# Performance work log

Hardware: AMD Instinct MI355X
Metric: run time of the kernel (lower is better)

Reference implementation:

```python
import jax, jax.numpy as jnp
import numpy as np
import math

B, S, DIM, HEADS, HEAD_DIM = 2, 2048, 1024, 16, 64
ROT_DIM, ROPE_THETA = 64, 10000.0


def make_rope(seq_len):
    # DitRotary.forward: theta over half rotary_dim, duplicated interleaved pairs
    theta = 1.0 / (ROPE_THETA ** (np.arange(0, ROT_DIM, 2, dtype=np.float32) / ROT_DIM))
    pos = np.arange(seq_len, dtype=np.float32).reshape(-1, 1)
    idx = pos * theta  # [S, 32]
    cos = np.stack((np.cos(idx), np.cos(idx)), axis=-1).reshape(seq_len, -1)  # [S, 64]
    sin = np.stack((np.sin(idx), np.sin(idx)), axis=-1).reshape(seq_len, -1)
    # unsqueeze(2).unsqueeze(1) -> [1, S, 1, 64]
    return jnp.asarray(cos)[None, :, None, :], jnp.asarray(sin)[None, :, None, :]


def rotate_half(x):
    # interleaved-pair rotation: (x1, x2) -> (-x2, x1)
    x = x.reshape(*x.shape[:-1], -1, 2)
    x1, x2 = x[..., 0], x[..., 1]
    return jnp.stack((-x2, x1), axis=-1).reshape(*x.shape[:-2], -1)


def apply_rotary(x, cos, sin):
    return x * cos + rotate_half(x) * sin


def setup_inputs() -> dict:
    key = jax.random.key(0)
    ks = jax.random.split(key, 8)
    sc = 1.0 / math.sqrt(DIM)
    x = jax.random.normal(ks[0], (B, S, DIM), dtype=jnp.float32)
    cos, sin = make_rope(S)
    Wq = jax.random.normal(ks[1], (DIM, DIM), dtype=jnp.float32) * sc
    bq = jnp.zeros((DIM,), jnp.float32)
    Wk = jax.random.normal(ks[2], (DIM, DIM), dtype=jnp.float32) * sc
    bk = jnp.zeros((DIM,), jnp.float32)
    Wv = jax.random.normal(ks[3], (DIM, DIM), dtype=jnp.float32) * sc
    bv = jnp.zeros((DIM,), jnp.float32)
    Wo = jax.random.normal(ks[4], (DIM, DIM), dtype=jnp.float32) * sc
    bo = jnp.zeros((DIM,), jnp.float32)
    mask = jnp.ones((B, 1, 1, S), dtype=bool)
    return {"x": x, "cos": cos, "sin": sin, "Wq": Wq, "bq": bq, "Wk": Wk,
            "bk": bk, "Wv": Wv, "bv": bv, "Wo": Wo, "bo": bo, "mask": mask}


def reference(x, cos, sin, Wq, bq, Wk, bk, Wv, bv, Wo, bo, mask):
    b, s, _ = x.shape
    q = (x @ Wq.T + bq).reshape(b, s, HEADS, HEAD_DIM)
    k = (x @ Wk.T + bk).reshape(b, s, HEADS, HEAD_DIM)
    v = (x @ Wv.T + bv).reshape(b, s, HEADS, HEAD_DIM)
    # partial rotary: applied only to head index 0 (dim 2 of [B,S,H,D])
    q = jnp.concatenate([apply_rotary(q[:, :, :1, :], cos, sin), q[:, :, 1:, :]], axis=2)
    k = jnp.concatenate([apply_rotary(k[:, :, :1, :], cos, sin), k[:, :, 1:, :]], axis=2)
    # [B,H,S,D]
    q = q.transpose(0, 2, 1, 3)
    k = k.transpose(0, 2, 1, 3)
    v = v.transpose(0, 2, 1, 3)
    neg = jnp.finfo(jnp.float32).min
    attn_mask = jnp.where(mask, 0.0, neg)  # ~mask * finfo.min
    scores = jnp.einsum("bhsd,bhtd->bhst", q, k) / math.sqrt(HEAD_DIM)
    scores = scores + attn_mask
    probs = jax.nn.softmax(scores.astype(jnp.float32), axis=-1).astype(q.dtype)
    out = jnp.einsum("bhst,bhtd->bhsd", probs, v)
    out = out.transpose(0, 2, 1, 3).reshape(b, s, HEADS * HEAD_DIM)
    return out @ Wo.T + bo
```

## Files before the change

### kernel.cpp

```cpp
#include <hip/hip_runtime.h>
#include <hip/hip_bf16.h>


typedef __attribute__((ext_vector_type(8))) __bf16 bf16x8;
typedef __attribute__((ext_vector_type(4))) __bf16 bf16x4;
typedef __attribute__((ext_vector_type(4))) float f32x4;
typedef __attribute__((ext_vector_type(4))) short s16x4;

#define NB_B 2
#define NB_S 2048
#define NB_DIM 1024
#define NB_H 16
#define NB_HD 64
#define NB_BS (NB_B * NB_S)

__device__ __forceinline__ void async_cp16(const __bf16* g, __bf16* l) {
    __builtin_amdgcn_global_load_lds(
        (const __attribute__((address_space(1))) unsigned int*)g,
        (__attribute__((address_space(3))) unsigned int*)l, 16, 0, 0);
}

__global__ __launch_bounds__(256) void cvt_kernel(
    const float* __restrict__ x,  const float* __restrict__ wq,
    const float* __restrict__ wk, const float* __restrict__ wv,
    const float* __restrict__ wo,
    __bf16* __restrict__ xb,  __bf16* __restrict__ wqb,
    __bf16* __restrict__ wkb, __bf16* __restrict__ wvb,
    __bf16* __restrict__ wob) {
    const int XQ = (NB_BS * NB_DIM) / 4;
    const int WQ = (NB_DIM * NB_DIM) / 4;
    int i = blockIdx.x * 256 + threadIdx.x;
    const float* src; __bf16* dst; int off;
    if (i < XQ)              { src = x;  dst = xb;  off = i; }
    else if (i < XQ + WQ)    { src = wq; dst = wqb; off = i - XQ; }
    else if (i < XQ + 2*WQ)  { src = wk; dst = wkb; off = i - XQ - WQ; }
    else if (i < XQ + 3*WQ)  { src = wv; dst = wvb; off = i - XQ - 2*WQ; }
    else                     { src = wo; dst = wob; off = i - XQ - 3*WQ; }
    f32x4 v = *(const f32x4*)(src + (size_t)off * 4);
    bf16x4 b;
#pragma unroll
    for (int j = 0; j < 4; ++j) b[j] = (__bf16)v[j];
    *(bf16x4*)(dst + (size_t)off * 4) = b;
}

__global__ __launch_bounds__(256) void gemm_qkv_kernel(
    const __bf16* __restrict__ A,
    const float* __restrict__ cosb, const float* __restrict__ sinb,
    const __bf16* __restrict__ Wq, const float* __restrict__ bq, __bf16* __restrict__ qbuf,
    const __bf16* __restrict__ Wk, const float* __restrict__ bk, __bf16* __restrict__ kbuf,
    const __bf16* __restrict__ Wv, const float* __restrict__ bv, __bf16* __restrict__ vtbuf) {
    constexpr int K = 1024;
    constexpr int NT = K / 32;
    __shared__ __align__(16) __bf16 As[3][128][32];
    __shared__ __align__(16) __bf16 Bs[3][128][32];

    const int z = blockIdx.z;
    const __bf16* W; const float* bias;
    if (z == 0)      { W = Wq; bias = bq; }
    else if (z == 1) { W = Wk; bias = bk; }
    else             { W = Wv; bias = bv; }

    const int tid = threadIdx.x;
    const int lane = tid & 63;
    const int w = tid >> 6;
    const int wm = w >> 1, wn = w & 1;
    const int row16 = lane & 15, quad = lane >> 4;
    const int m0 = blockIdx.x * 128, n0 = blockIdx.y * 128;

    f32x4 acc[4][4] = {};

    auto stage = [&](int nb, int kt) {
#pragma unroll
        for (int i = 0; i < 2; ++i) {
            int c = tid + i * 256;
            int row = c >> 2;
            int co = (c & 3) << 3;
            async_cp16(A + (size_t)(m0 + row) * K + kt + co, &As[nb][row][co]);
            async_cp16(W + (size_t)(n0 + row) * K + kt + co, &Bs[nb][row][co]);
        }
    };
    auto compute = [&](int nb) {
        bf16x8 af[4], bfr[4];
#pragma unroll
        for (int t = 0; t < 4; ++t) {
            af[t]  = *(const bf16x8*)&As[nb][wm * 64 + t * 16 + row16][quad * 8];
            bfr[t] = *(const bf16x8*)&Bs[nb][wn * 64 + t * 16 + row16][quad * 8];
        }
        __builtin_amdgcn_s_setprio(1);
#pragma unroll
        for (int mt = 0; mt < 4; ++mt)
#pragma unroll
            for (int nt = 0; nt < 4; ++nt)
                acc[mt][nt] = __builtin_amdgcn_mfma_f32_16x16x32_bf16(af[mt], bfr[nt], acc[mt][nt], 0, 0, 0);
        __builtin_amdgcn_s_setprio(0);
    };

    stage(0, 0);
    stage(1, 32);
    int cu = 0, pfb = 2;
    for (int t = 0; t < NT - 1; ++t) {
        asm volatile("s_waitcnt vmcnt(4)" ::: "memory");
        __builtin_amdgcn_s_barrier();
        if (t + 2 < NT) stage(pfb, (t + 2) * 32);
        compute(cu);
        cu  = (cu  == 2) ? 0 : cu + 1;
        pfb = (pfb == 2) ? 0 : pfb + 1;
    }
    asm volatile("s_waitcnt vmcnt(0)" ::: "memory");
    __builtin_amdgcn_s_barrier();
    compute(cu);

    if (z == 2) {
#pragma unroll
        for (int mt = 0; mt < 4; ++mt) {
            int row = m0 + wm * 64 + mt * 16 + quad * 4;
            int b = row >> 11, s = row & (NB_S - 1);
#pragma unroll
            for (int nt = 0; nt < 4; ++nt) {
                int col = n0 + wn * 64 + nt * 16 + row16;
                float bv = bias[col];
                bf16x4 pack;
#pragma unroll
                for (int r = 0; r < 4; ++r) pack[r] = (__bf16)(acc[mt][nt][r] + bv);
                *(bf16x4*)&vtbuf[(size_t)b * (NB_DIM * NB_S) + (size_t)col * NB_S + s] = pack;
            }
        }
    } else {
        __bf16* C = (z == 0) ? qbuf : kbuf;
        const bool rope = (n0 == 0) && (wn == 0);
#pragma unroll
        for (int mt = 0; mt < 4; ++mt) {
            int row = m0 + wm * 64 + mt * 16 + quad * 4;
#pragma unroll
            for (int nt = 0; nt < 4; ++nt) {
                int col = n0 + wn * 64 + nt * 16 + row16;
                float bv = bias[col];
#pragma unroll
                for (int r = 0; r < 4; ++r) {
                    float val = acc[mt][nt][r] + bv;
                    if (rope) {
                        float part = __shfl_xor(val, 1, 64);
                        int srow = (row + r) & (NB_S - 1);
                        float c  = cosb[srow * 64 + col];
                        float sn = sinb[srow * 64 + col];
                        val = (lane & 1) ? (val * c + part * sn) : (val * c - part * sn);
                    }
                    C[(size_t)(row + r) * NB_DIM + col] = (__bf16)val;
                }
            }
        }
    }
}

__global__ __launch_bounds__(256) void gemm_o_kernel(
    const __bf16* __restrict__ A, const __bf16* __restrict__ W,
    const float* __restrict__ bias, float* __restrict__ C) {
    constexpr int K = 1024;
    constexpr int NT = K / 32;
    __shared__ __align__(16) __bf16 As[3][128][32];
    __shared__ __align__(16) __bf16 Bs[3][64][32];

    const int tid = threadIdx.x;
    const int lane = tid & 63;
    const int w = tid >> 6;
    const int row16 = lane & 15, quad = lane >> 4;
    const int m0 = blockIdx.x * 128, n0 = blockIdx.y * 64;

    f32x4 acc[2][4] = {};

    auto stage = [&](int nb, int kt) {
#pragma unroll
        for (int i = 0; i < 2; ++i) {
            int c = tid + i * 256;
            int row = c >> 2;
            int co = (c & 3) << 3;
            async_cp16(A + (size_t)(m0 + row) * K + kt + co, &As[nb][row][co]);
        }
        {
            int row = tid >> 2;
            int co = (tid & 3) << 3;
            async_cp16(W + (size_t)(n0 + row) * K + kt + co, &Bs[nb][row][co]);
        }
    };
    auto compute = [&](int nb) {
        bf16x8 af[2], bfr[4];
#pragma unroll
        for (int t = 0; t < 2; ++t)
            af[t] = *(const bf16x8*)&As[nb][w * 32 + t * 16 + row16][quad * 8];
#pragma unroll
        for (int nt = 0; nt < 4; ++nt)
            bfr[nt] = *(const bf16x8*)&Bs[nb][nt * 16 + row16][quad * 8];
        __builtin_amdgcn_s_setprio(1);
#pragma unroll
        for (int mt = 0; mt < 2; ++mt)
#pragma unroll
            for (int nt = 0; nt < 4; ++nt)
                acc[mt][nt] = __builtin_amdgcn_mfma_f32_16x16x32_bf16(af[mt], bfr[nt], acc[mt][nt], 0, 0, 0);
        __builtin_amdgcn_s_setprio(0);
    };

    stage(0, 0);
    stage(1, 32);
    int cu = 0, pfb = 2;
    for (int t = 0; t < NT - 1; ++t) {
        asm volatile("s_waitcnt vmcnt(3)" ::: "memory");
        __builtin_amdgcn_s_barrier();
        if (t + 2 < NT) stage(pfb, (t + 2) * 32);
        compute(cu);
        cu  = (cu  == 2) ? 0 : cu + 1;
        pfb = (pfb == 2) ? 0 : pfb + 1;
    }
    asm volatile("s_waitcnt vmcnt(0)" ::: "memory");
    __builtin_amdgcn_s_barrier();
    compute(cu);

#pragma unroll
    for (int mt = 0; mt < 2; ++mt) {
        int row = m0 + w * 32 + mt * 16 + quad * 4;
#pragma unroll
        for (int nt = 0; nt < 4; ++nt) {
            int col = n0 + nt * 16 + row16;
            float bv = bias[col];
#pragma unroll
            for (int r = 0; r < 4; ++r)
                C[(size_t)(row + r) * NB_DIM + col] = acc[mt][nt][r] + bv;
        }
    }
}

__global__ __launch_bounds__(256) void attn_kernel(const __bf16* __restrict__ qb,
                                                   const __bf16* __restrict__ kb,
                                                   const __bf16* __restrict__ vtb,
                                                   __bf16* __restrict__ ob) {
    __shared__ __align__(16) __bf16 Ks[128][72];
    __shared__ __align__(16) __bf16 Vts[64][132];

    const int tid = threadIdx.x;
    const int lane = tid & 63;
    const int w = tid >> 6;
    const int row16 = lane & 15, quad = lane >> 4;
    const int bh = blockIdx.y;
    const int b = bh >> 4, h = bh & 15;
    const int q0 = blockIdx.x * 128 + w * 32;

    const size_t headoff = (size_t)b * NB_S * NB_DIM + (size_t)h * NB_HD;
    const size_t vtoff = (size_t)b * (NB_DIM * NB_S) + (size_t)(h * NB_HD) * NB_S;

    const float qscale = 0.18033688011112042f;
    bf16x8 qf[2][2];
#pragma unroll
    for (int m = 0; m < 2; ++m)
#pragma unroll
        for (int hh = 0; hh < 2; ++hh) {
            bf16x8 v = *(const bf16x8*)(qb + headoff + (size_t)(q0 + m * 16 + row16) * NB_DIM + hh * 32 + quad * 8);
#pragma unroll
            for (int j = 0; j < 8; ++j) v[j] = (__bf16)((float)v[j] * qscale);
            qf[m][hh] = v;
        }

    f32x4 o[2][4] = {};
    f32x4 ol[2] = {};

    const short one_bf16 = (short)0x3F80;
    const s16x4 onesf = {one_bf16, one_bf16, one_bf16, one_bf16};

    bf16x8 kreg[4], vreg[4];
#pragma unroll
    for (int i = 0; i < 4; ++i) {
        int c = tid + i * 256;
        kreg[i] = *(const bf16x8*)(kb + headoff + (size_t)(c >> 3) * NB_DIM + ((c & 7) << 3));
        vreg[i] = *(const bf16x8*)(vtb + vtoff + (size_t)(c >> 4) * NB_S + ((c & 15) << 3));
    }

    for (int kt = 0; kt < 16; ++kt) {
        __syncthreads();
#pragma unroll
        for (int i = 0; i < 4; ++i) {
            int c = tid + i * 256;
            *(bf16x8*)&Ks[c >> 3][(c & 7) << 3] = kreg[i];
            bf16x4 lo, hi;
#pragma unroll
            for (int j = 0; j < 4; ++j) { lo[j] = vreg[i][j]; hi[j] = vreg[i][j + 4]; }
            *(bf16x4*)&Vts[c >> 4][(c & 15) << 3] = lo;
            *(bf16x4*)&Vts[c >> 4][((c & 15) << 3) + 4] = hi;
        }
        __syncthreads();
        if (kt < 15) {
            int base = (kt + 1) * 128;
#pragma unroll
            for (int i = 0; i < 4; ++i) {
                int c = tid + i * 256;
                kreg[i] = *(const bf16x8*)(kb + headoff + (size_t)(base + (c >> 3)) * NB_DIM + ((c & 7) << 3));
                vreg[i] = *(const bf16x8*)(vtb + vtoff + (size_t)(c >> 4) * NB_S + base + ((c & 15) << 3));
            }
        }

        s16x4 pf[2][8];
#pragma unroll
        for (int t = 0; t < 8; ++t) {
            f32x4 s0 = {}, s1 = {};
            __builtin_amdgcn_s_setprio(1);
#pragma unroll
            for (int hh = 0; hh < 2; ++hh) {
                bf16x8 kf = *(const bf16x8*)&Ks[t * 16 + row16][hh * 32 + quad * 8];
                s0 = __builtin_amdgcn_mfma_f32_16x16x32_bf16(kf, qf[0][hh], s0, 0, 0, 0);
                s1 = __builtin_amdgcn_mfma_f32_16x16x32_bf16(kf, qf[1][hh], s1, 0, 0, 0);
            }
            __builtin_amdgcn_s_setprio(0);
            bf16x4 p0, p1;
#pragma unroll
            for (int r = 0; r < 4; ++r) {
                float e0 = __builtin_amdgcn_exp2f(s0[r]); p0[r] = (__bf16)e0;
                float e1 = __builtin_amdgcn_exp2f(s1[r]); p1[r] = (__bf16)e1;
            }
            pf[0][t] = __builtin_bit_cast(s16x4, p0);
            pf[1][t] = __builtin_bit_cast(s16x4, p1);
            ol[0] = __builtin_amdgcn_mfma_f32_16x16x16bf16_1k(pf[0][t], onesf, ol[0], 0, 0, 0);
            ol[1] = __builtin_amdgcn_mfma_f32_16x16x16bf16_1k(pf[1][t], onesf, ol[1], 0, 0, 0);
        }

        __builtin_amdgcn_s_setprio(1);
#pragma unroll
        for (int nt = 0; nt < 4; ++nt)
#pragma unroll
            for (int t = 0; t < 8; ++t) {
                s16x4 vf = *(const s16x4*)&Vts[nt * 16 + row16][t * 16 + quad * 4];
                o[0][nt] = __builtin_amdgcn_mfma_f32_16x16x16bf16_1k(pf[0][t], vf, o[0][nt], 0, 0, 0);
                o[1][nt] = __builtin_amdgcn_mfma_f32_16x16x16bf16_1k(pf[1][t], vf, o[1][nt], 0, 0, 0);
            }
        __builtin_amdgcn_s_setprio(0);
    }

#pragma unroll
    for (int m = 0; m < 2; ++m)
#pragma unroll
        for (int r = 0; r < 4; ++r) {
            float inv = 1.f / ol[m][r];
            int row = q0 + m * 16 + quad * 4 + r;
#pragma unroll
            for (int nt = 0; nt < 4; ++nt)
                ob[headoff + (size_t)row * NB_DIM + nt * 16 + row16] = (__bf16)(o[m][nt][r] * inv);
        }
}

extern "C" void kernel_launch(void* const* d_in, const int* in_sizes, int n_in,
                              void* d_out, int out_size, void* d_ws, size_t ws_size,
                              hipStream_t stream) {
    const float* x    = (const float*)d_in[0];
    const float* cosb = (const float*)d_in[1];
    const float* sinb = (const float*)d_in[2];
    const float* Wq   = (const float*)d_in[3];
    const float* bq   = (const float*)d_in[4];
    const float* Wk   = (const float*)d_in[5];
    const float* bk   = (const float*)d_in[6];
    const float* Wv   = (const float*)d_in[7];
    const float* bv   = (const float*)d_in[8];
    const float* Wo   = (const float*)d_in[9];
    const float* bo   = (const float*)d_in[10];

    __bf16* qbuf  = (__bf16*)d_ws;
    __bf16* kbuf  = qbuf + (size_t)NB_BS * NB_DIM;
    __bf16* vtbuf = kbuf + (size_t)NB_BS * NB_DIM;
    __bf16* abuf  = vtbuf + (size_t)NB_BS * NB_DIM;
    __bf16* xb    = abuf + (size_t)NB_BS * NB_DIM;
    __bf16* wqb   = xb + (size_t)NB_BS * NB_DIM;
    __bf16* wkb   = wqb + (size_t)NB_DIM * NB_DIM;
    __bf16* wvb   = wkb + (size_t)NB_DIM * NB_DIM;
    __bf16* wob   = wvb + (size_t)NB_DIM * NB_DIM;

    const int XQ = (NB_BS * NB_DIM) / 4, WQ = (NB_DIM * NB_DIM) / 4;
    cvt_kernel<<<(XQ + 4 * WQ) / 256, 256, 0, stream>>>(x, Wq, Wk, Wv, Wo,
                                                        xb, wqb, wkb, wvb, wob);

    dim3 gqkv(NB_BS / 128, NB_DIM / 128, 3);
    gemm_qkv_kernel<<<gqkv, 256, 0, stream>>>(xb, cosb, sinb,
                                              wqb, bq, qbuf,
                                              wkb, bk, kbuf,
                                              wvb, bv, vtbuf);

    attn_kernel<<<dim3(NB_S / 128, NB_B * NB_H), 256, 0, stream>>>(qbuf, kbuf, vtbuf, abuf);

    dim3 go(NB_BS / 128, NB_DIM / 64);
    gemm_o_kernel<<<go, 256, 0, stream>>>(abuf, wob, bo, (float*)d_out);
}
```

Baseline: 211.6 us.

## Use single-buffered swizzled K64 tiles in QKV GEMM and 8-wave attention blocks

Measured after the change: 208.1 us. About the same (-1.7%).

```diff
diff --git a/kernel.cpp b/kernel.cpp
--- a/kernel.cpp
+++ b/kernel.cpp
@@ -50,9 +50,8 @@
     const __bf16* __restrict__ Wk, const float* __restrict__ bk, __bf16* __restrict__ kbuf,
     const __bf16* __restrict__ Wv, const float* __restrict__ bv, __bf16* __restrict__ vtbuf) {
     constexpr int K = 1024;
-    constexpr int NT = K / 32;
-    __shared__ __align__(16) __bf16 As[3][128][32];
-    __shared__ __align__(16) __bf16 Bs[3][128][32];
+    __shared__ __align__(16) __bf16 As[128][64];
+    __shared__ __align__(16) __bf16 Bs[128][64];
 
     const int z = blockIdx.z;
     const __bf16* W; const float* bias;
@@ -65,50 +64,41 @@
     const int w = tid >> 6;
     const int wm = w >> 1, wn = w & 1;
     const int row16 = lane & 15, quad = lane >> 4;
+    const int r7 = row16 & 7;
     const int m0 = blockIdx.x * 128, n0 = blockIdx.y * 128;
 
     f32x4 acc[4][4] = {};
 
-    auto stage = [&](int nb, int kt) {
-#pragma unroll
-        for (int i = 0; i < 2; ++i) {
+    for (int kt = 0; kt < K; kt += 64) {
+        __syncthreads();
+#pragma unroll
+        for (int i = 0; i < 4; ++i) {
             int c = tid + i * 256;
-            int row = c >> 2;
-            int co = (c & 3) << 3;
-            async_cp16(A + (size_t)(m0 + row) * K + kt + co, &As[nb][row][co]);
-            async_cp16(W + (size_t)(n0 + row) * K + kt + co, &Bs[nb][row][co]);
-        }
-    };
-    auto compute = [&](int nb) {
-        bf16x8 af[4], bfr[4];
-#pragma unroll
-        for (int t = 0; t < 4; ++t) {
-            af[t]  = *(const bf16x8*)&As[nb][wm * 64 + t * 16 + row16][quad * 8];
-            bfr[t] = *(const bf16x8*)&Bs[nb][wn * 64 + t * 16 + row16][quad * 8];
-        }
+            int row = c >> 3, g = c & 7;
+            int gcol = (g ^ (row & 7)) << 3;
+            async_cp16(A + (size_t)(m0 + row) * K + kt + gcol, &As[row][g << 3]);
+            async_cp16(W + (size_t)(n0 + row) * K + kt + gcol, &Bs[row][g << 3]);
+        }
+        __syncthreads();
+
+        bf16x8 af[4][2], bfr[4][2];
+#pragma unroll
+        for (int t = 0; t < 4; ++t)
+#pragma unroll
+            for (int kk = 0; kk < 2; ++kk) {
+                af[t][kk]  = *(const bf16x8*)&As[wm * 64 + t * 16 + row16][((kk * 4 + quad) ^ r7) << 3];
+                bfr[t][kk] = *(const bf16x8*)&Bs[wn * 64 + t * 16 + row16][((kk * 4 + quad) ^ r7) << 3];
+            }
         __builtin_amdgcn_s_setprio(1);
 #pragma unroll
         for (int mt = 0; mt < 4; ++mt)
 #pragma unroll
             for (int nt = 0; nt < 4; ++nt)
-                acc[mt][nt] = __builtin_amdgcn_mfma_f32_16x16x32_bf16(af[mt], bfr[nt], acc[mt][nt], 0, 0, 0);
+#pragma unroll
+                for (int kk = 0; kk < 2; ++kk)
+                    acc[mt][nt] = __builtin_amdgcn_mfma_f32_16x16x32_bf16(af[mt][kk], bfr[nt][kk], acc[mt][nt], 0, 0, 0);
         __builtin_amdgcn_s_setprio(0);
-    };
-
-    stage(0, 0);
-    stage(1, 32);
-    int cu = 0, pfb = 2;
-    for (int t = 0; t < NT - 1; ++t) {
-        asm volatile("s_waitcnt vmcnt(4)" ::: "memory");
-        __builtin_amdgcn_s_barrier();
-        if (t + 2 < NT) stage(pfb, (t + 2) * 32);
-        compute(cu);
-        cu  = (cu  == 2) ? 0 : cu + 1;
-        pfb = (pfb == 2) ? 0 : pfb + 1;
-    }
-    asm volatile("s_waitcnt vmcnt(0)" ::: "memory");
-    __builtin_amdgcn_s_barrier();
-    compute(cu);
+    }
 
     if (z == 2) {
 #pragma unroll
@@ -228,7 +218,7 @@
     }
 }
 
-__global__ __launch_bounds__(256) void attn_kernel(const __bf16* __restrict__ qb,
+__global__ __launch_bounds__(512) void attn_kernel(const __bf16* __restrict__ qb,
                                                    const __bf16* __restrict__ kb,
                                                    const __bf16* __restrict__ vtb,
                                                    __bf16* __restrict__ ob) {
@@ -241,33 +231,31 @@
     const int row16 = lane & 15, quad = lane >> 4;
     const int bh = blockIdx.y;
     const int b = bh >> 4, h = bh & 15;
-    const int q0 = blockIdx.x * 128 + w * 32;
+    const int q0 = blockIdx.x * 128 + w * 16;
 
     const size_t headoff = (size_t)b * NB_S * NB_DIM + (size_t)h * NB_HD;
     const size_t vtoff = (size_t)b * (NB_DIM * NB_S) + (size_t)(h * NB_HD) * NB_S;
 
     const float qscale = 0.18033688011112042f;
-    bf16x8 qf[2][2];
-#pragma unroll
-    for (int m = 0; m < 2; ++m)
-#pragma unroll
-        for (int hh = 0; hh < 2; ++hh) {
-            bf16x8 v = *(const bf16x8*)(qb + headoff + (size_t)(q0 + m * 16 + row16) * NB_DIM + hh * 32 + quad * 8);
-#pragma unroll
-            for (int j = 0; j < 8; ++j) v[j] = (__bf16)((float)v[j] * qscale);
-            qf[m][hh] = v;
-        }
-
-    f32x4 o[2][4] = {};
-    f32x4 ol[2] = {};
+    bf16x8 qf[2];
+#pragma unroll
+    for (int hh = 0; hh < 2; ++hh) {
+        bf16x8 v = *(const bf16x8*)(qb + headoff + (size_t)(q0 + row16) * NB_DIM + hh * 32 + quad * 8);
+#pragma unroll
+        for (int j = 0; j < 8; ++j) v[j] = (__bf16)((float)v[j] * qscale);
+        qf[hh] = v;
+    }
+
+    f32x4 o[4] = {};
+    f32x4 ol = {};
 
     const short one_bf16 = (short)0x3F80;
     const s16x4 onesf = {one_bf16, one_bf16, one_bf16, one_bf16};
 
-    bf16x8 kreg[4], vreg[4];
-#pragma unroll
-    for (int i = 0; i < 4; ++i) {
-        int c = tid + i * 256;
+    bf16x8 kreg[2], vreg[2];
+#pragma unroll
+    for (int i = 0; i < 2; ++i) {
+        int c = tid + i * 512;
         kreg[i] = *(const bf16x8*)(kb + headoff + (size_t)(c >> 3) * NB_DIM + ((c & 7) << 3));
         vreg[i] = *(const bf16x8*)(vtb + vtoff + (size_t)(c >> 4) * NB_S + ((c & 15) << 3));
     }
@@ -275,8 +263,8 @@
     for (int kt = 0; kt < 16; ++kt) {
         __syncthreads();
 #pragma unroll
-        for (int i = 0; i < 4; ++i) {
-            int c = tid + i * 256;
+        for (int i = 0; i < 2; ++i) {
+            int c = tid + i * 512;
             *(bf16x8*)&Ks[c >> 3][(c & 7) << 3] = kreg[i];
             bf16x4 lo, hi;
 #pragma unroll
@@ -288,35 +276,32 @@
         if (kt < 15) {
             int base = (kt + 1) * 128;
 #pragma unroll
-            for (int i = 0; i < 4; ++i) {
-                int c = tid + i * 256;
+            for (int i = 0; i < 2; ++i) {
+                int c = tid + i * 512;
                 kreg[i] = *(const bf16x8*)(kb + headoff + (size_t)(base + (c >> 3)) * NB_DIM + ((c & 7) << 3));
                 vreg[i] = *(const bf16x8*)(vtb + vtoff + (size_t)(c >> 4) * NB_S + base + ((c & 15) << 3));
             }
         }
 
-        s16x4 pf[2][8];
+        s16x4 pf[8];
 #pragma unroll
         for (int t = 0; t < 8; ++t) {
-            f32x4 s0 = {}, s1 = {};
+            f32x4 s = {};
             __builtin_amdgcn_s_setprio(1);
 #pragma unroll
             for (int hh = 0; hh < 2; ++hh) {
                 bf16x8 kf = *(const bf16x8*)&Ks[t * 16 + row16][hh * 32 + quad * 8];
-                s0 = __builtin_amdgcn_mfma_f32_16x16x32_bf16(kf, qf[0][hh], s0, 0, 0, 0);
-                s1 = __builtin_amdgcn_mfma_f32_16x16x32_bf16(kf, qf[1][hh], s1, 0, 0, 0);
+                s = __builtin_amdgcn_mfma_f32_16x16x32_bf16(kf, qf[hh], s, 0, 0, 0);
             }
             __builtin_amdgcn_s_setprio(0);
-            bf16x4 p0, p1;
+            bf16x4 p;
 #pragma unroll
             for (int r = 0; r < 4; ++r) {
-                float e0 = __builtin_amdgcn_exp2f(s0[r]); p0[r] = (__bf16)e0;
-                float e1 = __builtin_amdgcn_exp2f(s1[r]); p1[r] = (__bf16)e1;
-            }
-            pf[0][t] = __builtin_bit_cast(s16x4, p0);
-            pf[1][t] = __builtin_bit_cast(s16x4, p1);
-            ol[0] = __builtin_amdgcn_mfma_f32_16x16x16bf16_1k(pf[0][t], onesf, ol[0], 0, 0, 0);
-            ol[1] = __builtin_amdgcn_mfma_f32_16x16x16bf16_1k(pf[1][t], onesf, ol[1], 0, 0, 0);
+                float e = __builtin_amdgcn_exp2f(s[r]);
+                p[r] = (__bf16)e;
+            }
+            pf[t] = __builtin_bit_cast(s16x4, p);
+            ol = __builtin_amdgcn_mfma_f32_16x16x16bf16_1k(pf[t], onesf, ol, 0, 0, 0);
         }
 
         __builtin_amdgcn_s_setprio(1);
@@ -325,22 +310,19 @@
 #pragma unroll
             for (int t = 0; t < 8; ++t) {
                 s16x4 vf = *(const s16x4*)&Vts[nt * 16 + row16][t * 16 + quad * 4];
-                o[0][nt] = __builtin_amdgcn_mfma_f32_16x16x16bf16_1k(pf[0][t], vf, o[0][nt], 0, 0, 0);
-                o[1][nt] = __builtin_amdgcn_mfma_f32_16x16x16bf16_1k(pf[1][t], vf, o[1][nt], 0, 0, 0);
+                o[nt] = __builtin_amdgcn_mfma_f32_16x16x16bf16_1k(pf[t], vf, o[nt], 0, 0, 0);
             }
         __builtin_amdgcn_s_setprio(0);
     }
 
 #pragma unroll
-    for (int m = 0; m < 2; ++m)
-#pragma unroll
-        for (int r = 0; r < 4; ++r) {
-            float inv = 1.f / ol[m][r];
-            int row = q0 + m * 16 + quad * 4 + r;
-#pragma unroll
-            for (int nt = 0; nt < 4; ++nt)
-                ob[headoff + (size_t)row * NB_DIM + nt * 16 + row16] = (__bf16)(o[m][nt][r] * inv);
-        }
+    for (int r = 0; r < 4; ++r) {
+        float inv = 1.f / ol[r];
+        int row = q0 + quad * 4 + r;
+#pragma unroll
+        for (int nt = 0; nt < 4; ++nt)
+            ob[headoff + (size_t)row * NB_DIM + nt * 16 + row16] = (__bf16)(o[nt][r] * inv);
+    }
 }
 
 extern "C" void kernel_launch(void* const* d_in, const int* in_sizes, int n_in,
@@ -378,7 +360,7 @@
                                               wkb, bk, kbuf,
                                               wvb, bv, vtbuf);
 
-    attn_kernel<<<dim3(NB_S / 128, NB_B * NB_H), 256, 0, stream>>>(qbuf, kbuf, vtbuf, abuf);
+    attn_kernel<<<dim3(NB_S / 128, NB_B * NB_H), 512, 0, stream>>>(qbuf, kbuf, vtbuf, abuf);
 
     dim3 go(NB_BS / 128, NB_DIM / 64);
     gemm_o_kernel<<<go, 256, 0, stream>>>(abuf, wob, bo, (float*)d_out);
```
